# Performance work log

Hardware: AMD Instinct MI355X
Metric: run time of the kernel (lower is better)

Reference implementation:

```python
import jax, jax.numpy as jnp
import numpy as np

N_NODES = 100000
DIM = 128
BATCH = 50000
K = 10  # num_sample


def setup_inputs() -> dict:
    key = jax.random.key(0)
    k1, k2, k3 = jax.random.split(key, 3)
    nodes = jax.random.randint(k1, (BATCH,), 0, N_NODES, dtype=jnp.int64 if jax.config.jax_enable_x64 else jnp.int32)
    neighbours = jax.random.randint(k2, (BATCH, K), 0, N_NODES, dtype=nodes.dtype)
    features = jax.random.normal(k3, (N_NODES, DIM), dtype=jnp.float32)
    return {"nodes": nodes, "neighbours": neighbours, "features": features}


def reference(nodes, neighbours, features):
    # Mean over each node's neighborhood union {self}: gather K neighbor rows
    # plus the self row and average over K+1 members. Equivalent to the
    # row-normalized 0/1 mask GEMM in the original (assuming distinct ids).
    feat_nb = features[neighbours]          # [B, K, D]
    feat_self = features[nodes]             # [B, D]
    denom = jnp.asarray(K + 1, features.dtype)
    return (feat_nb.sum(axis=1) + feat_self) / denom  # [B, D]
```

## Files before the change

### kernel.cpp

```cpp
#include <hip/hip_runtime.h>
#include <hip/hip_fp16.h>


#define B_BATCH 50000
#define K_NB 10
#define DIM 128
#define N_NODES 100000
#define F4_PER_ROW (DIM / 4)
#define U4_PER_ROW (DIM / 8)

__global__ __launch_bounds__(256)
void convert_fp16_kernel(const float* __restrict__ in, __half2* __restrict__ out)
{
    const size_t total_f4 = (size_t)N_NODES * DIM / 4;
    size_t i = (size_t)blockIdx.x * 256 + threadIdx.x;
    if (i >= total_f4) return;
    float4 v = reinterpret_cast<const float4*>(in)[i];
    out[2 * i]     = __floats2half2_rn(v.x, v.y);
    out[2 * i + 1] = __floats2half2_rn(v.z, v.w);
}

__global__ __launch_bounds__(256)
void mean_agg_fp16_kernel(const int* __restrict__ nodes,
                          const int* __restrict__ neighbours,
                          const __half* __restrict__ feat,
                          float* __restrict__ out)
{
    const int row  = blockIdx.x * 16 + (threadIdx.x >> 4);
    if (row >= B_BATCH) return;
    const int lane = threadIdx.x & 15;

    int idx[K_NB + 1];
    idx[0] = nodes[row];
#pragma unroll
    for (int j = 0; j < K_NB; ++j)
        idx[j + 1] = neighbours[row * K_NB + j];

    const uint4* __restrict__ f4 = reinterpret_cast<const uint4*>(feat);

    uint4 v[K_NB + 1];
#pragma unroll
    for (int j = 0; j < K_NB + 1; ++j)
        v[j] = f4[(size_t)idx[j] * U4_PER_ROW + lane];

    float acc[8] = {0.f, 0.f, 0.f, 0.f, 0.f, 0.f, 0.f, 0.f};
#pragma unroll
    for (int j = 0; j < K_NB + 1; ++j) {
        const __half2* h = reinterpret_cast<const __half2*>(&v[j]);
#pragma unroll
        for (int q = 0; q < 4; ++q) {
            float2 f = __half22float2(h[q]);
            acc[2 * q]     += f.x;
            acc[2 * q + 1] += f.y;
        }
    }
    const float s = 1.0f / (float)(K_NB + 1);
#pragma unroll
    for (int q = 0; q < 8; ++q) acc[q] *= s;

    float4* o4 = reinterpret_cast<float4*>(out) + (size_t)row * F4_PER_ROW + lane * 2;
    o4[0] = make_float4(acc[0], acc[1], acc[2], acc[3]);
    o4[1] = make_float4(acc[4], acc[5], acc[6], acc[7]);
}

__global__ __launch_bounds__(256)
void mean_agg_fp32_kernel(const int* __restrict__ nodes,
                          const int* __restrict__ neighbours,
                          const float* __restrict__ features,
                          float* __restrict__ out)
{
    const int row  = blockIdx.x * 8 + (threadIdx.x >> 5);
    if (row >= B_BATCH) return;
    const int lane = threadIdx.x & 31;

    int idx[K_NB + 1];
    idx[0] = nodes[row];
#pragma unroll
    for (int j = 0; j < K_NB; ++j)
        idx[j + 1] = neighbours[row * K_NB + j];

    const float4* __restrict__ f4 = reinterpret_cast<const float4*>(features);
    float4 v[K_NB + 1];
#pragma unroll
    for (int j = 0; j < K_NB + 1; ++j)
        v[j] = f4[(size_t)idx[j] * F4_PER_ROW + lane];

    float4 acc = v[0];
#pragma unroll
    for (int j = 1; j < K_NB + 1; ++j) {
        acc.x += v[j].x; acc.y += v[j].y; acc.z += v[j].z; acc.w += v[j].w;
    }
    const float s = 1.0f / (float)(K_NB + 1);
    acc.x *= s; acc.y *= s; acc.z *= s; acc.w *= s;
    reinterpret_cast<float4*>(out)[(size_t)row * F4_PER_ROW + lane] = acc;
}

extern "C" void kernel_launch(void* const* d_in, const int* in_sizes, int n_in,
                              void* d_out, int out_size, void* d_ws, size_t ws_size,
                              hipStream_t stream)
{
    const int*   nodes      = (const int*)d_in[0];
    const int*   neighbours = (const int*)d_in[1];
    const float* features   = (const float*)d_in[2];
    float*       out        = (float*)d_out;

    const size_t fp16_bytes = (size_t)N_NODES * DIM * sizeof(__half);

    if (ws_size >= fp16_bytes) {
        __half* feat16 = (__half*)d_ws;
        const size_t total_f4 = (size_t)N_NODES * DIM / 4;
        const int conv_grid = (int)((total_f4 + 255) / 256);
        convert_fp16_kernel<<<conv_grid, 256, 0, stream>>>(features, (__half2*)feat16);
        const int gather_grid = (B_BATCH + 15) / 16;
        mean_agg_fp16_kernel<<<gather_grid, 256, 0, stream>>>(nodes, neighbours, feat16, out);
    } else {
        const int gather_grid = (B_BATCH + 7) / 8;
        mean_agg_fp32_kernel<<<gather_grid, 256, 0, stream>>>(nodes, neighbours, features, out);
    }
}
```

Before: 115.9 us.

## Split fp16 feature table into column chunks for cache-local gathers

Measured after the change: 131.5 us. +13.5%, slower.

```diff
diff --git a/kernel.cpp b/kernel.cpp
--- a/kernel.cpp
+++ b/kernel.cpp
@@ -6,50 +6,66 @@
 #define K_NB 10
 #define DIM 128
 #define N_NODES 100000
+#define CHUNKS 8
+#define CDIM 16
 #define F4_PER_ROW (DIM / 4)
-#define U4_PER_ROW (DIM / 8)
+
+typedef float  fx4 __attribute__((ext_vector_type(4)));
 
 __global__ __launch_bounds__(256)
-void convert_fp16_kernel(const float* __restrict__ in, __half2* __restrict__ out)
+void convert_chunk_kernel(const float* __restrict__ in, __half* __restrict__ ws)
 {
-    const size_t total_f4 = (size_t)N_NODES * DIM / 4;
-    size_t i = (size_t)blockIdx.x * 256 + threadIdx.x;
-    if (i >= total_f4) return;
-    float4 v = reinterpret_cast<const float4*>(in)[i];
-    out[2 * i]     = __floats2half2_rn(v.x, v.y);
-    out[2 * i + 1] = __floats2half2_rn(v.z, v.w);
+    const int total = N_NODES * CHUNKS;
+    int t = blockIdx.x * 256 + threadIdx.x;
+    if (t >= total) return;
+    const int n = t >> 3;
+    const int c = t & 7;
+
+    const float4* src = reinterpret_cast<const float4*>(in) + (size_t)t * 4;
+    float4 a = src[0], b = src[1], d = src[2], e = src[3];
+
+    __half2 h[8];
+    h[0] = __floats2half2_rn(a.x, a.y); h[1] = __floats2half2_rn(a.z, a.w);
+    h[2] = __floats2half2_rn(b.x, b.y); h[3] = __floats2half2_rn(b.z, b.w);
+    h[4] = __floats2half2_rn(d.x, d.y); h[5] = __floats2half2_rn(d.z, d.w);
+    h[6] = __floats2half2_rn(e.x, e.y); h[7] = __floats2half2_rn(e.z, e.w);
+
+    uint4* dst = reinterpret_cast<uint4*>(ws + ((size_t)c * N_NODES + n) * CDIM);
+    dst[0] = *reinterpret_cast<uint4*>(&h[0]);
+    dst[1] = *reinterpret_cast<uint4*>(&h[4]);
 }
 
 __global__ __launch_bounds__(256)
-void mean_agg_fp16_kernel(const int* __restrict__ nodes,
-                          const int* __restrict__ neighbours,
-                          const __half* __restrict__ feat,
-                          float* __restrict__ out)
+void gather_chunk_kernel(const int* __restrict__ nodes,
+                         const int* __restrict__ neighbours,
+                         const __half* __restrict__ ws,
+                         float* __restrict__ out)
 {
-    const int row  = blockIdx.x * 16 + (threadIdx.x >> 4);
+    const int c   = blockIdx.x & 7;
+    const int row = (blockIdx.x >> 3) * 128 + (threadIdx.x >> 1);
     if (row >= B_BATCH) return;
-    const int lane = threadIdx.x & 15;
+    const int h   = threadIdx.x & 1;
 
     int idx[K_NB + 1];
-    idx[0] = nodes[row];
+    idx[0] = __builtin_nontemporal_load(nodes + row);
 #pragma unroll
     for (int j = 0; j < K_NB; ++j)
-        idx[j + 1] = neighbours[row * K_NB + j];
+        idx[j + 1] = __builtin_nontemporal_load(neighbours + row * K_NB + j);
 
-    const uint4* __restrict__ f4 = reinterpret_cast<const uint4*>(feat);
+    const uint4* base = reinterpret_cast<const uint4*>(ws + (size_t)c * N_NODES * CDIM) + h;
 
     uint4 v[K_NB + 1];
 #pragma unroll
     for (int j = 0; j < K_NB + 1; ++j)
-        v[j] = f4[(size_t)idx[j] * U4_PER_ROW + lane];
+        v[j] = base[(size_t)idx[j] * 2];
 
     float acc[8] = {0.f, 0.f, 0.f, 0.f, 0.f, 0.f, 0.f, 0.f};
 #pragma unroll
     for (int j = 0; j < K_NB + 1; ++j) {
-        const __half2* h = reinterpret_cast<const __half2*>(&v[j]);
+        const __half2* p = reinterpret_cast<const __half2*>(&v[j]);
 #pragma unroll
         for (int q = 0; q < 4; ++q) {
-            float2 f = __half22float2(h[q]);
+            float2 f = __half22float2(p[q]);
             acc[2 * q]     += f.x;
             acc[2 * q + 1] += f.y;
         }
@@ -58,9 +74,11 @@
 #pragma unroll
     for (int q = 0; q < 8; ++q) acc[q] *= s;
 
-    float4* o4 = reinterpret_cast<float4*>(out) + (size_t)row * F4_PER_ROW + lane * 2;
-    o4[0] = make_float4(acc[0], acc[1], acc[2], acc[3]);
-    o4[1] = make_float4(acc[4], acc[5], acc[6], acc[7]);
+    float* o = out + (size_t)row * DIM + c * CDIM + h * 8;
+    fx4 r0 = {acc[0], acc[1], acc[2], acc[3]};
+    fx4 r1 = {acc[4], acc[5], acc[6], acc[7]};
+    __builtin_nontemporal_store(r0, reinterpret_cast<fx4*>(o));
+    __builtin_nontemporal_store(r1, reinterpret_cast<fx4*>(o) + 1);
 }
 
 __global__ __launch_bounds__(256)
@@ -108,11 +126,13 @@
 
     if (ws_size >= fp16_bytes) {
         __half* feat16 = (__half*)d_ws;
-        const size_t total_f4 = (size_t)N_NODES * DIM / 4;
-        const int conv_grid = (int)((total_f4 + 255) / 256);
-        convert_fp16_kernel<<<conv_grid, 256, 0, stream>>>(features, (__half2*)feat16);
-        const int gather_grid = (B_BATCH + 15) / 16;
-        mean_agg_fp16_kernel<<<gather_grid, 256, 0, stream>>>(nodes, neighbours, feat16, out);
+
+        const int conv_threads = N_NODES * CHUNKS;
+        const int conv_grid = (conv_threads + 255) / 256;
+        convert_chunk_kernel<<<conv_grid, 256, 0, stream>>>(features, feat16);
+
+        const int row_blocks = (B_BATCH + 127) / 128;
+        gather_chunk_kernel<<<row_blocks * CHUNKS, 256, 0, stream>>>(nodes, neighbours, feat16, out);
     } else {
         const int gather_grid = (B_BATCH + 7) / 8;
         mean_agg_fp32_kernel<<<gather_grid, 256, 0, stream>>>(nodes, neighbours, features, out);
```
